# Kernel optimization log

Measured on AMD Instinct MI355X. Metric: run time of the kernel, lower is better.

## Reference

```python
import jax, jax.numpy as jnp
import numpy as np

B, H, W, D = 16, 32, 32, 256
K = 8192


def setup_inputs() -> dict:
    key = jax.random.key(0)
    k1, k2 = jax.random.split(key)
    z_e = jax.random.normal(k1, (B, H, W, D), dtype=jnp.float32)
    # flax nn.initializers.uniform(scale=1.0) -> U[0, 1)
    codebook = jax.random.uniform(k2, (K, D), dtype=jnp.float32)
    return {"z_e": z_e, "codebook": codebook}


def reference(z_e, codebook):
    b, h, w, d = z_e.shape
    z_flat = z_e.reshape(-1, d)  # (N, D)
    # squared-euclidean distances: ||z||^2 + ||e||^2 - 2 z.e  -> (N, K)
    z2 = jnp.sum(z_flat ** 2, axis=1, keepdims=True)
    e2 = jnp.sum(codebook ** 2, axis=1)[None, :]
    dist = z2 + e2 - 2.0 * (z_flat @ codebook.T)
    idx = jnp.argmin(dist, axis=1)  # (N,)
    z_q = codebook[idx].reshape(b, h, w, d)
    # straight-through estimator
    z_st = z_e + jax.lax.stop_gradient(z_q - z_e)
    commit = jnp.mean((jax.lax.stop_gradient(z_q) - z_e) ** 2)
    codebook_loss = jnp.mean((z_q - jax.lax.stop_gradient(z_e)) ** 2)
    return z_st, idx.reshape(b, h, w), commit, codebook_loss
```

## Files before the change

kernel.cpp:

```cpp
#include <hip/hip_runtime.h>

#define NROWS 16384
#define KCODES 8192
#define DDIM 256
#define MARGIN 1.0f
#define SEG 192
#define NCT 16
#define GATHER_BLOCKS (NROWS / 16)

typedef __attribute__((ext_vector_type(8))) short short8;
typedef __attribute__((ext_vector_type(4))) float f32x4;

__device__ inline unsigned short f2bf(float x) {
    unsigned u = __float_as_uint(x);
    return (unsigned short)((u + 0x7FFFu + ((u >> 16) & 1u)) >> 16);
}

__device__ inline unsigned mbcnt64(unsigned long long m) {
    unsigned lo = __builtin_amdgcn_mbcnt_lo((unsigned)m, 0u);
    return __builtin_amdgcn_mbcnt_hi((unsigned)(m >> 32), lo);
}

__device__ inline void exact_rescore(const float* __restrict__ z, const float* __restrict__ cb,
                                     const float* __restrict__ z2g, const float* __restrict__ e2g,
                                     int grow, int gcol, unsigned long long* best) {
    const float4* av = reinterpret_cast<const float4*>(z + (size_t)grow * DDIM);
    const float4* bv = reinterpret_cast<const float4*>(cb + (size_t)gcol * DDIM);
    float dot = 0.f;
    #pragma unroll 8
    for (int j = 0; j < 64; ++j) {
        const float4 xa = av[j], xb = bv[j];
        dot = fmaf(xa.x, xb.x, fmaf(xa.y, xb.y, fmaf(xa.z, xb.z, fmaf(xa.w, xb.w, dot))));
    }
    const float de = z2g[grow] + e2g[gcol] - 2.0f * dot;
    const unsigned long long key =
        ((unsigned long long)__float_as_uint(de) << 32) | (unsigned)gcol;
    atomicMin(best + grow, key);
}

__global__ __launch_bounds__(256) void k_convert(
    const float* __restrict__ cb, unsigned short* __restrict__ cb_t,
    float* __restrict__ e2,
    unsigned long long* best, float* accum, unsigned* counters, unsigned* gctr)
{
    const int tid = threadIdx.x;
    const int bx = blockIdx.x;
    if (bx < 64) {
        const int gid = bx * 256 + tid;
        best[gid] = 0xFFFFFFFFFFFFFFFFull;
    }
    if (bx == 0) {
        if (tid < 16) counters[tid * 16] = 0u;
        if (tid == 0) { accum[0] = 0.0f; gctr[0] = 0u; }
    }
    const int g = bx * 4 + (tid >> 6);
    const int lane = tid & 63;
    const int row = g * 16 + (lane & 15);
    const int ko = (lane >> 4) * 8;
    float ss = 0.f;
    #pragma unroll
    for (int kb2 = 0; kb2 < 8; ++kb2) {
        const float4* src = reinterpret_cast<const float4*>(cb + (size_t)row * DDIM + kb2 * 32 + ko);
        const float4 a = src[0], b = src[1];
        ss += a.x * a.x + a.y * a.y + a.z * a.z + a.w * a.w
            + b.x * b.x + b.y * b.y + b.z * b.z + b.w * b.w;
        short8 p;
        p[0] = (short)f2bf(a.x); p[1] = (short)f2bf(a.y); p[2] = (short)f2bf(a.z); p[3] = (short)f2bf(a.w);
        p[4] = (short)f2bf(b.x); p[5] = (short)f2bf(b.y); p[6] = (short)f2bf(b.z); p[7] = (short)f2bf(b.w);
        *reinterpret_cast<short8*>(cb_t + (((size_t)(g * 8 + kb2)) << 9) + lane * 8) = p;
    }
    ss += __shfl_xor(ss, 16);
    ss += __shfl_xor(ss, 32);
    if (lane < 16) e2[g * 16 + lane] = ss;
}

__global__ __launch_bounds__(1024, 4) void k_screen(
    const float* __restrict__ z, const float* __restrict__ cbp,
    const unsigned short* __restrict__ cb_t,
    float* z2g, const float* __restrict__ e2g,
    unsigned long long* __restrict__ best,
    unsigned* __restrict__ counters, unsigned* __restrict__ list, unsigned C16)
{
    __shared__ __align__(16) char smem[47360];
    char* ldsA = smem;
    float* rowmin = (float*)(smem + 32768);
    float* thrbuf = (float*)(smem + 34816);
    unsigned* wl_all = (unsigned*)(smem + 35072);

    const int tid = threadIdx.x;
    const int lane = tid & 63;
    const int wave = tid >> 6;
    const int wm = wave & 1;
    const int wn = wave >> 1;
    const int lhi = lane >> 4;
    const int llo = lane & 15;

    const int rt = blockIdx.x;
    const int row0 = rt * 64;

    {
        const int c = tid >> 5;
        const int gl = c >> 3, kb2 = c & 7;
        const int sp = (tid & 31) * 2;
        #pragma unroll
        for (int i = 0; i < 2; ++i) {
            const int s = sp + i;
            const int row = gl * 16 + (s & 15);
            const int k = kb2 * 32 + (s >> 4) * 8;
            const float4* src = reinterpret_cast<const float4*>(z + (size_t)(row0 + row) * DDIM + k);
            const float4 a = src[0], b = src[1];
            short8 p;
            p[0] = (short)f2bf(a.x); p[1] = (short)f2bf(a.y); p[2] = (short)f2bf(a.z); p[3] = (short)f2bf(a.w);
            p[4] = (short)f2bf(b.x); p[5] = (short)f2bf(b.y); p[6] = (short)f2bf(b.z); p[7] = (short)f2bf(b.w);
            *reinterpret_cast<short8*>(ldsA + c * 1024 + s * 16) = p;
        }
    }

    #pragma unroll
    for (int rr = 0; rr < 4; ++rr) {
        const int row = wave * 4 + rr;
        const float4 v = *reinterpret_cast<const float4*>(z + (size_t)(row0 + row) * DDIM + lane * 4);
        float s = v.x * v.x + v.y * v.y + v.z * v.z + v.w * v.w;
        #pragma unroll
        for (int off = 1; off < 64; off <<= 1) s += __shfl_xor(s, off);
        if (lane == 0) z2g[row0 + row] = s;
    }

    if (tid < 64) thrbuf[tid] = 3.0e38f;
    __syncthreads();

    unsigned* wl = wl_all + wave * SEG;

    #pragma unroll 1
    for (int ci = 0; ci < NCT; ++ci) {
        f32x4 acc[2][4];
        #pragma unroll
        for (int i = 0; i < 2; ++i)
            #pragma unroll
            for (int j = 0; j < 4; ++j) { acc[i][j][0]=0.f; acc[i][j][1]=0.f; acc[i][j][2]=0.f; acc[i][j][3]=0.f; }

        const char* bbase = (const char*)cb_t + (((size_t)((ci * 32 + wn * 4)) * 8) << 10) + lane * 16;
        #pragma unroll
        for (int kb2 = 0; kb2 < 8; ++kb2) {
            short8 bfr[4];
            #pragma unroll
            for (int fn = 0; fn < 4; ++fn)
                bfr[fn] = *reinterpret_cast<const short8*>(bbase + fn * 8192 + kb2 * 1024);
            #pragma unroll
            for (int fm = 0; fm < 2; ++fm) {
                const short8 af = *reinterpret_cast<const short8*>(
                    ldsA + (((wm * 2 + fm) * 8) + kb2) * 1024 + lane * 16);
                #pragma unroll
                for (int fn = 0; fn < 4; ++fn)
                    acc[fm][fn] = __builtin_amdgcn_mfma_f32_16x16x32_bf16(af, bfr[fn], acc[fm][fn], 0, 0, 0);
            }
        }

        const int c0 = ci * 512 + wn * 64 + llo;
        float e2c[4];
        #pragma unroll
        for (int fn = 0; fn < 4; ++fn) e2c[fn] = e2g[c0 + fn * 16];

        #pragma unroll
        for (int fm = 0; fm < 2; ++fm) {
            #pragma unroll
            for (int rg = 0; rg < 4; ++rg) {
                const int rl = wm * 32 + fm * 16 + lhi * 4 + rg;
                float d[4];
                #pragma unroll
                for (int fn = 0; fn < 4; ++fn) d[fn] = fmaf(-2.0f, acc[fm][fn][rg], e2c[fn]);
                float m = fminf(fminf(d[0], d[1]), fminf(d[2], d[3]));
                #pragma unroll
                for (int off = 1; off < 16; off <<= 1) m = fminf(m, __shfl_xor(m, off));
                if (llo == 0) rowmin[wn * 64 + rl] = m;
            }
        }
        asm volatile("s_waitcnt lgkmcnt(0)" ::: "memory");
        __builtin_amdgcn_s_barrier();
        __builtin_amdgcn_sched_barrier(0);

        if (tid < 64) {
            float a = rowmin[tid];
            #pragma unroll
            for (int q = 1; q < 8; ++q) a = fminf(a, rowmin[q * 64 + tid]);
            thrbuf[tid] = fminf(thrbuf[tid], a);
        }
        asm volatile("s_waitcnt lgkmcnt(0)" ::: "memory");
        __builtin_amdgcn_s_barrier();
        __builtin_amdgcn_sched_barrier(0);

        unsigned wcount = 0;
        #pragma unroll
        for (int fm = 0; fm < 2; ++fm) {
            #pragma unroll
            for (int rg = 0; rg < 4; ++rg) {
                const int rl = wm * 32 + fm * 16 + lhi * 4 + rg;
                const float thr = thrbuf[rl] + MARGIN;
                float d[4];
                #pragma unroll
                for (int fn = 0; fn < 4; ++fn) d[fn] = fmaf(-2.0f, acc[fm][fn][rg], e2c[fn]);
                const bool hit = (d[0] <= thr) | (d[1] <= thr) | (d[2] <= thr) | (d[3] <= thr);
                if (__any(hit)) {
                    const int grow = row0 + rl;
                    #pragma unroll
                    for (int fn = 0; fn < 4; ++fn) {
                        const bool p = d[fn] <= thr;
                        const unsigned long long mask = __ballot(p);
                        if (mask) {
                            if (p) {
                                const unsigned pos = wcount + mbcnt64(mask);
                                const unsigned v = ((unsigned)grow << 13) | (unsigned)(c0 + fn * 16);
                                if (pos < SEG) wl[pos] = v;
                                else exact_rescore(z, cbp, z2g, e2g, grow, c0 + fn * 16, best);
                            }
                            wcount += (unsigned)__popcll(mask);
                        }
                    }
                }
            }
        }

        const unsigned n = wcount < SEG ? wcount : SEG;
        unsigned base = 0;
        if (lane == 0 && n) base = atomicAdd(&counters[wave * 16], n);
        base = (unsigned)__shfl((int)base, 0);
        for (unsigned i = lane; i < n; i += 64) {
            const unsigned v = wl[i];
            const unsigned slot = base + i;
            if (slot < C16) list[(size_t)wave * C16 + slot] = v;
            else exact_rescore(z, cbp, z2g, e2g, (int)(v >> 13), (int)(v & 8191u), best);
        }
    }
}

__global__ __launch_bounds__(256) void k_rescore(
    const float* __restrict__ z, const float* __restrict__ cbp,
    const float* __restrict__ z2g, const float* __restrict__ e2g,
    const unsigned* __restrict__ list, const unsigned* __restrict__ counters, unsigned C16,
    unsigned long long* best)
{
    const unsigned wid = (blockIdx.x * blockDim.x + threadIdx.x) >> 6;
    const unsigned nw = (gridDim.x * blockDim.x) >> 6;
    const int lane = threadIdx.x & 63;
    #pragma unroll 1
    for (int s = 0; s < 16; ++s) {
        const unsigned n = min(counters[s * 16], C16);
        const unsigned* shard = list + (size_t)s * C16;
        for (unsigned i = wid; i < n; i += nw) {
            const unsigned v = shard[i];
            const unsigned row = v >> 13, col = v & 8191u;
            const float4 a = *reinterpret_cast<const float4*>(z + (size_t)row * DDIM + lane * 4);
            const float4 b = *reinterpret_cast<const float4*>(cbp + (size_t)col * DDIM + lane * 4);
            float sdot = fmaf(a.x, b.x, fmaf(a.y, b.y, fmaf(a.z, b.z, a.w * b.w)));
            #pragma unroll
            for (int off = 1; off < 64; off <<= 1) sdot += __shfl_xor(sdot, off);
            if (lane == 0) {
                const float de = z2g[row] + e2g[col] - 2.0f * sdot;
                const unsigned long long key =
                    ((unsigned long long)__float_as_uint(de) << 32) | col;
                atomicMin(&best[row], key);
            }
        }
    }
}

__global__ __launch_bounds__(1024) void k_gather(
    const float* __restrict__ z, const float* __restrict__ cbp,
    const unsigned long long* __restrict__ best,
    float* __restrict__ out, float* __restrict__ accum, unsigned* __restrict__ gctr)
{
    __shared__ float wsum[16];
    const int tid = threadIdx.x;
    const int row = blockIdx.x * 16 + (tid >> 6);
    const int lane = tid & 63;
    const unsigned k = (unsigned)(best[row] & 0xFFFFFFFFull);
    const float4 ze = *reinterpret_cast<const float4*>(z + (size_t)row * DDIM + lane * 4);
    const float4 cq = *reinterpret_cast<const float4*>(cbp + (size_t)k * DDIM + lane * 4);
    float4 zst;
    zst.x = ze.x + (cq.x - ze.x); zst.y = ze.y + (cq.y - ze.y);
    zst.z = ze.z + (cq.z - ze.z); zst.w = ze.w + (cq.w - ze.w);
    *reinterpret_cast<float4*>(out + (size_t)row * DDIM + lane * 4) = zst;
    const float dx = cq.x - ze.x, dy = cq.y - ze.y, dz = cq.z - ze.z, dw = cq.w - ze.w;
    float s = dx * dx + dy * dy + dz * dz + dw * dw;
    #pragma unroll
    for (int off = 32; off > 0; off >>= 1) s += __shfl_down(s, off);
    if (lane == 0) {
        wsum[tid >> 6] = s;
        out[(size_t)NROWS * DDIM + row] = (float)k;
    }
    __syncthreads();
    if (tid == 0) {
        float tot = 0.f;
        #pragma unroll
        for (int i = 0; i < 16; ++i) tot += wsum[i];
        atomicAdd(accum, tot);
        __threadfence();
        const unsigned t = atomicAdd(gctr, 1u);
        if (t == GATHER_BLOCKS - 1) {
            const float total = atomicAdd(accum, 0.0f);
            const float m = total / (float)(NROWS * DDIM);
            out[(size_t)NROWS * DDIM + NROWS + 0] = m;
            out[(size_t)NROWS * DDIM + NROWS + 1] = m;
        }
    }
}

extern "C" void kernel_launch(void* const* d_in, const int* in_sizes, int n_in,
                              void* d_out, int out_size, void* d_ws, size_t ws_size,
                              hipStream_t stream)
{
    const float* z  = (const float*)d_in[0];
    const float* cb = (const float*)d_in[1];
    float* out = (float*)d_out;

    unsigned short* cb_t = (unsigned short*)d_out;

    char* ws = (char*)d_ws;
    unsigned long long* best = (unsigned long long*)ws;
    float* e2      = (float*)(ws + 131072);
    float* z2      = (float*)(ws + 163840);
    float* accum   = (float*)(ws + 229376);
    unsigned* gctr = (unsigned*)(ws + 229380);
    unsigned* counters = (unsigned*)(ws + 229440);
    unsigned* list = (unsigned*)(ws + 230464);
    unsigned C16 = 0;
    if (ws_size > 230464 + 64) {
        size_t c = (ws_size - 230464) / 4 / 16;
        if (c > (1u << 19)) c = (1u << 19);
        C16 = (unsigned)c;
    }

    k_convert<<<128, 256, 0, stream>>>(cb, cb_t, e2, best, accum, counters, gctr);
    k_screen<<<256, 1024, 0, stream>>>(z, cb, cb_t, z2, e2, best, counters, list, C16);
    k_rescore<<<1024, 256, 0, stream>>>(z, cb, z2, e2, list, counters, C16, best);
    k_gather<<<GATHER_BLOCKS, 1024, 0, stream>>>(z, cb, best, out, accum, gctr);
}
```

Measured before the change: 210.0 us.

## Split screen kernel across codebook halves and double-buffer codebook fragment loads

The screening kernel now launches 512 blocks of 512 threads, each block covering one 64-row tile against half of the codebook, which doubles the number of blocks for better CU occupancy. The B-fragment global loads are double-buffered so that the next k-slice loads while MFMAs run on the current one, and MFMA sections get raised wave priority. Each block still converts its own z rows to bf16 in LDS, so this conversion and the z2 computation are now done twice. The shared-memory layout, row-min reduction and candidate shard indexing are adjusted to match.

```diff
diff --git a/kernel.cpp b/kernel.cpp
--- a/kernel.cpp
+++ b/kernel.cpp
@@ -74,18 +74,18 @@
     if (lane < 16) e2[g * 16 + lane] = ss;
 }
 
-__global__ __launch_bounds__(1024, 4) void k_screen(
+__global__ __launch_bounds__(512, 4) void k_screen(
     const float* __restrict__ z, const float* __restrict__ cbp,
     const unsigned short* __restrict__ cb_t,
     float* z2g, const float* __restrict__ e2g,
     unsigned long long* __restrict__ best,
     unsigned* __restrict__ counters, unsigned* __restrict__ list, unsigned C16)
 {
-    __shared__ __align__(16) char smem[47360];
+    __shared__ __align__(16) char smem[40192];
     char* ldsA = smem;
     float* rowmin = (float*)(smem + 32768);
-    float* thrbuf = (float*)(smem + 34816);
-    unsigned* wl_all = (unsigned*)(smem + 35072);
+    float* thrbuf = (float*)(smem + 33792);
+    unsigned* wl_all = (unsigned*)(smem + 34048);
 
     const int tid = threadIdx.x;
     const int lane = tid & 63;
@@ -95,15 +95,17 @@
     const int lhi = lane >> 4;
     const int llo = lane & 15;
 
-    const int rt = blockIdx.x;
+    const int bx = blockIdx.x;
+    const int rt = bx & 255;
+    const int cgrp = bx >> 8;
     const int row0 = rt * 64;
 
     {
-        const int c = tid >> 5;
+        const int c = tid >> 4;
         const int gl = c >> 3, kb2 = c & 7;
-        const int sp = (tid & 31) * 2;
-        #pragma unroll
-        for (int i = 0; i < 2; ++i) {
+        const int sp = (tid & 15) * 4;
+        #pragma unroll
+        for (int i = 0; i < 4; ++i) {
             const int s = sp + i;
             const int row = gl * 16 + (s & 15);
             const int k = kb2 * 32 + (s >> 4) * 8;
@@ -115,21 +117,31 @@
             *reinterpret_cast<short8*>(ldsA + c * 1024 + s * 16) = p;
         }
     }
-
     #pragma unroll
-    for (int rr = 0; rr < 4; ++rr) {
-        const int row = wave * 4 + rr;
+    for (int rr = 0; rr < 8; ++rr) {
+        const int row = wave * 8 + rr;
         const float4 v = *reinterpret_cast<const float4*>(z + (size_t)(row0 + row) * DDIM + lane * 4);
         float s = v.x * v.x + v.y * v.y + v.z * v.z + v.w * v.w;
         #pragma unroll
         for (int off = 1; off < 64; off <<= 1) s += __shfl_xor(s, off);
         if (lane == 0) z2g[row0 + row] = s;
     }
-
     if (tid < 64) thrbuf[tid] = 3.0e38f;
     __syncthreads();
 
     unsigned* wl = wl_all + wave * SEG;
+
+    auto LOADB = [&](short8* dst, int ci_, int kb2_) {
+        const char* base = (const char*)cb_t +
+            ((((size_t)(cgrp * 256 + ci_ * 16 + wn * 4)) * 8 + kb2_) << 10) + lane * 16;
+        dst[0] = *reinterpret_cast<const short8*>(base);
+        dst[1] = *reinterpret_cast<const short8*>(base + 8192);
+        dst[2] = *reinterpret_cast<const short8*>(base + 16384);
+        dst[3] = *reinterpret_cast<const short8*>(base + 24576);
+    };
+
+    short8 bA[4], bB[4];
+    LOADB(bA, 0, 0);
 
     #pragma unroll 1
     for (int ci = 0; ci < NCT; ++ci) {
@@ -139,24 +151,36 @@
             #pragma unroll
             for (int j = 0; j < 4; ++j) { acc[i][j][0]=0.f; acc[i][j][1]=0.f; acc[i][j][2]=0.f; acc[i][j][3]=0.f; }
 
-        const char* bbase = (const char*)cb_t + (((size_t)((ci * 32 + wn * 4)) * 8) << 10) + lane * 16;
-        #pragma unroll
-        for (int kb2 = 0; kb2 < 8; ++kb2) {
-            short8 bfr[4];
-            #pragma unroll
-            for (int fn = 0; fn < 4; ++fn)
-                bfr[fn] = *reinterpret_cast<const short8*>(bbase + fn * 8192 + kb2 * 1024);
+        #pragma unroll
+        for (int kp = 0; kp < 4; ++kp) {
+            const int ke = kp * 2;
+            LOADB(bB, ci, ke + 1);
+            __builtin_amdgcn_s_setprio(1);
             #pragma unroll
             for (int fm = 0; fm < 2; ++fm) {
                 const short8 af = *reinterpret_cast<const short8*>(
-                    ldsA + (((wm * 2 + fm) * 8) + kb2) * 1024 + lane * 16);
+                    ldsA + (((wm * 2 + fm) * 8) + ke) * 1024 + lane * 16);
                 #pragma unroll
                 for (int fn = 0; fn < 4; ++fn)
-                    acc[fm][fn] = __builtin_amdgcn_mfma_f32_16x16x32_bf16(af, bfr[fn], acc[fm][fn], 0, 0, 0);
-            }
-        }
-
-        const int c0 = ci * 512 + wn * 64 + llo;
+                    acc[fm][fn] = __builtin_amdgcn_mfma_f32_16x16x32_bf16(af, bA[fn], acc[fm][fn], 0, 0, 0);
+            }
+            __builtin_amdgcn_s_setprio(0);
+            const int ko_ = ke + 1;
+            if (ko_ < 7) LOADB(bA, ci, ko_ + 1);
+            else if (ci < NCT - 1) LOADB(bA, ci + 1, 0);
+            __builtin_amdgcn_s_setprio(1);
+            #pragma unroll
+            for (int fm = 0; fm < 2; ++fm) {
+                const short8 af = *reinterpret_cast<const short8*>(
+                    ldsA + (((wm * 2 + fm) * 8) + ko_) * 1024 + lane * 16);
+                #pragma unroll
+                for (int fn = 0; fn < 4; ++fn)
+                    acc[fm][fn] = __builtin_amdgcn_mfma_f32_16x16x32_bf16(af, bB[fn], acc[fm][fn], 0, 0, 0);
+            }
+            __builtin_amdgcn_s_setprio(0);
+        }
+
+        const int c0 = cgrp * 4096 + ci * 256 + wn * 64 + llo;
         float e2c[4];
         #pragma unroll
         for (int fn = 0; fn < 4; ++fn) e2c[fn] = e2g[c0 + fn * 16];
@@ -180,9 +204,8 @@
         __builtin_amdgcn_sched_barrier(0);
 
         if (tid < 64) {
-            float a = rowmin[tid];
-            #pragma unroll
-            for (int q = 1; q < 8; ++q) a = fminf(a, rowmin[q * 64 + tid]);
+            float a = fminf(fminf(rowmin[tid], rowmin[64 + tid]),
+                            fminf(rowmin[128 + tid], rowmin[192 + tid]));
             thrbuf[tid] = fminf(thrbuf[tid], a);
         }
         asm volatile("s_waitcnt lgkmcnt(0)" ::: "memory");
@@ -221,13 +244,14 @@
         }
 
         const unsigned n = wcount < SEG ? wcount : SEG;
+        const int sh = (bx & 1) * 8 + wave;
         unsigned base = 0;
-        if (lane == 0 && n) base = atomicAdd(&counters[wave * 16], n);
+        if (lane == 0 && n) base = atomicAdd(&counters[sh * 16], n);
         base = (unsigned)__shfl((int)base, 0);
         for (unsigned i = lane; i < n; i += 64) {
             const unsigned v = wl[i];
             const unsigned slot = base + i;
-            if (slot < C16) list[(size_t)wave * C16 + slot] = v;
+            if (slot < C16) list[(size_t)sh * C16 + slot] = v;
             else exact_rescore(z, cbp, z2g, e2g, (int)(v >> 13), (int)(v & 8191u), best);
         }
     }
@@ -331,7 +355,7 @@
     }
 
     k_convert<<<128, 256, 0, stream>>>(cb, cb_t, e2, best, accum, counters, gctr);
-    k_screen<<<256, 1024, 0, stream>>>(z, cb, cb_t, z2, e2, best, counters, list, C16);
+    k_screen<<<512, 512, 0, stream>>>(z, cb, cb_t, z2, e2, best, counters, list, C16);
     k_rescore<<<1024, 256, 0, stream>>>(z, cb, z2, e2, list, counters, C16, best);
     k_gather<<<GATHER_BLOCKS, 1024, 0, stream>>>(z, cb, best, out, accum, gctr);
 }
```

After: 254.5 us. 21.2% more time.
